# Performance work log

Hardware: AMD Instinct MI355X
Metric: run time of the kernel (lower is better)

Reference implementation:

```python
import jax, jax.numpy as jnp
import numpy as np

N_HEADS = 16
KQ_DIM = 64
EMB_DIM = 1024
CTX_DIM = 1024
EPS = 1e-5

def _layernorm(x, w, b):
    # LayerNorm over last dim (kq_dim), elementwise affine
    mu = jnp.mean(x, axis=-1, keepdims=True)
    var = jnp.mean(jnp.square(x - mu), axis=-1, keepdims=True)
    return (x - mu) * jax.lax.rsqrt(var + EPS) * w + b

def setup_inputs() -> dict:
    key = jax.random.key(0)
    ks = jax.random.split(key, 10)
    B, SQ, SK = 2, 2048, 2048
    inner = N_HEADS * KQ_DIM
    s_e = 1.0 / np.sqrt(EMB_DIM)
    s_c = 1.0 / np.sqrt(CTX_DIM)
    s_i = 1.0 / np.sqrt(inner)
    return {
        "emb": jax.random.normal(ks[0], (B, SQ, EMB_DIM), jnp.float32),
        "context": jax.random.normal(ks[1], (B, SK, CTX_DIM), jnp.float32),
        "Wq": jax.random.uniform(ks[2], (inner, EMB_DIM), jnp.float32, -s_e, s_e),
        "Wk": jax.random.uniform(ks[3], (inner, CTX_DIM), jnp.float32, -s_c, s_c),
        "Wv": jax.random.uniform(ks[4], (inner, CTX_DIM), jnp.float32, -s_c, s_c),
        "Wu": jax.random.uniform(ks[5], (EMB_DIM, inner), jnp.float32, -s_i, s_i),
        "bu": jax.random.uniform(ks[6], (EMB_DIM,), jnp.float32, -s_i, s_i),
        "qn_w": jnp.ones((KQ_DIM,), jnp.float32),
        "qn_b": jnp.zeros((KQ_DIM,), jnp.float32),
        "kn_w": jnp.ones((KQ_DIM,), jnp.float32),
        "kn_b": jnp.zeros((KQ_DIM,), jnp.float32),
    }

def reference(emb, context, Wq, Wk, Wv, Wu, bu, qn_w, qn_b, kn_w, kn_b):
    B, SQ, _ = emb.shape
    SK = context.shape[1]
    # projections (no bias), reshape to [B, H, S, D]
    q = (emb @ Wq.T).reshape(B, SQ, N_HEADS, KQ_DIM).transpose(0, 2, 1, 3)
    k = (context @ Wk.T).reshape(B, SK, N_HEADS, KQ_DIM).transpose(0, 2, 1, 3)
    v = (context @ Wv.T).reshape(B, SK, N_HEADS, KQ_DIM).transpose(0, 2, 1, 3)
    q = _layernorm(q, qn_w, qn_b)
    k = _layernorm(k, kn_w, kn_b)
    scale = 1.0 / jnp.sqrt(jnp.asarray(KQ_DIM, emb.dtype))
    attn = jnp.einsum('bhqd,bhkd->bhqk', q, k) * scale
    attn = jax.nn.softmax(attn, axis=-1)
    out = jnp.einsum('bhqk,bhkd->bhqd', attn, v)
    out = out.transpose(0, 2, 1, 3).reshape(B, SQ, N_HEADS * KQ_DIM)
    return out @ Wu.T + bu
```

## Files before the change

kernel.cpp:

```cpp
#include <hip/hip_runtime.h>


typedef __attribute__((ext_vector_type(8)))  short bf16x8;
typedef __attribute__((ext_vector_type(4)))  short bf16x4;
typedef __attribute__((ext_vector_type(4)))  float f32x4;
typedef __attribute__((ext_vector_type(16))) float f32x16;
typedef __attribute__((ext_vector_type(4)))  unsigned int u32x4;

typedef __attribute__((address_space(1))) const void cg_void;
typedef __attribute__((address_space(3))) void lds_void_t;

__device__ __forceinline__ void gl_lds16(const void* g, void* l){
  __builtin_amdgcn_global_load_lds((cg_void*)g, (lds_void_t*)l, 16, 0, 0);
}

__device__ __forceinline__ short f2b(float f){
  unsigned int u;
  __builtin_memcpy(&u, &f, 4);
  u += 0x7fffu + ((u >> 16) & 1u);
  return (short)(u >> 16);
}

__global__ __launch_bounds__(256) void cvt6_kernel(
    const float* __restrict__ emb, const float* __restrict__ ctx,
    const float* __restrict__ Wq, const float* __restrict__ Wk,
    const float* __restrict__ Wv, const float* __restrict__ Wu,
    short* __restrict__ o_emb, short* __restrict__ o_ctx,
    short* __restrict__ o_wq, short* __restrict__ o_wk,
    short* __restrict__ o_wv, short* __restrict__ o_wu)
{
  const long M1 = 1024L * 1024L, M4 = 4L * M1;
  long e = ((long)blockIdx.x * 256 + threadIdx.x) * 4;
  if (e >= 12L * M1) return;
  const float* src; short* dst; long off;
  if      (e <     M4)      { src = emb; dst = o_emb; off = e;           }
  else if (e < 2 * M4)      { src = ctx; dst = o_ctx; off = e - M4;      }
  else if (e < 2 * M4 + M1) { src = Wq;  dst = o_wq;  off = e - 2 * M4;  }
  else if (e < 2 * M4 + 2*M1){src = Wk;  dst = o_wk;  off = e - 2*M4 - M1;}
  else if (e < 2 * M4 + 3*M1){src = Wv;  dst = o_wv;  off = e - 2*M4 - 2*M1;}
  else                      { src = Wu;  dst = o_wu;  off = e - 2*M4 - 3*M1;}
  f32x4 v = *(const f32x4*)(src + off);
  bf16x4 o;
  o[0] = f2b(v[0]); o[1] = f2b(v[1]); o[2] = f2b(v[2]); o[3] = f2b(v[3]);
  *(bf16x4*)(dst + off) = o;
}

__global__ __launch_bounds__(256) void gemm_qkv_kernel(
    const short* __restrict__ embh, const short* __restrict__ ctxh,
    const short* __restrict__ Wqh, const short* __restrict__ Wkh,
    const short* __restrict__ Wvh,
    short* __restrict__ qo, short* __restrict__ ko, short* __restrict__ vto,
    const float* __restrict__ qw, const float* __restrict__ qb,
    const float* __restrict__ kw, const float* __restrict__ kb)
{
  const int K = 1024;
  __shared__ short As[128 * 64];
  __shared__ short Bs[128 * 64];
  const int tid  = threadIdx.x;
  const int wave = tid >> 6, lane = tid & 63;
  const int quad = lane >> 4, r16 = lane & 15;
  const int wm = (wave >> 1) * 64, wn = (wave & 1) * 64;

  const int task = blockIdx.y;
  int bn, bm, N;
  const short *A, *B;
  if (task == 2){
    bn = (blockIdx.x & 31) * 128; bm = (blockIdx.x >> 5) * 128; N = 4096;
    A = Wvh; B = ctxh;
  } else {
    bm = (blockIdx.x & 31) * 128; bn = (blockIdx.x >> 5) * 128; N = 1024;
    A = task ? ctxh : embh; B = task ? Wkh : Wqh;
  }

  f32x4 acc[4][4];
#pragma unroll
  for (int i = 0; i < 4; i++)
#pragma unroll
    for (int j = 0; j < 4; j++)
      acc[i][j] = (f32x4){0.f, 0.f, 0.f, 0.f};

  const int sr7 = (lane >> 3) & 7;
  const size_t arow = (size_t)(bm + wave * 8 + (lane >> 3)) * K
                      + (((lane & 7) ^ sr7) * 8);
  const size_t brow = (size_t)(bn + wave * 8 + (lane >> 3)) * K
                      + (((lane & 7) ^ sr7) * 8);

  const int sw = ((quad ^ (r16 & 7)) << 3);

  for (int k0 = 0; k0 < K; k0 += 64){
#pragma unroll
    for (int i = 0; i < 4; i++){
      gl_lds16(A + arow + (size_t)32 * i * K + k0, &As[wave * 512 + i * 2048]);
      gl_lds16(B + brow + (size_t)32 * i * K + k0, &Bs[wave * 512 + i * 2048]);
    }
    __syncthreads();
#pragma unroll
    for (int kk = 0; kk < 2; kk++){
      const int off = sw ^ (kk << 5);
      bf16x8 af[4], bq[4];
#pragma unroll
      for (int i = 0; i < 4; i++)
        af[i] = *(const bf16x8*)(&As[(wm + i*16 + r16) * 64 + off]);
#pragma unroll
      for (int j = 0; j < 4; j++)
        bq[j] = *(const bf16x8*)(&Bs[(wn + j*16 + r16) * 64 + off]);
#pragma unroll
      for (int i = 0; i < 4; i++)
#pragma unroll
        for (int j = 0; j < 4; j++)
          acc[i][j] = __builtin_amdgcn_mfma_f32_16x16x32_bf16(af[i], bq[j], acc[i][j], 0, 0, 0);
    }
    __syncthreads();
  }

  if (task < 2){
    short* Ch = task ? ko : qo;
    const float* lw = task ? kw : qw;
    const float* lb = task ? kb : qb;
    float wv[4], bv[4];
#pragma unroll
    for (int j = 0; j < 4; j++){ wv[j] = lw[j*16 + r16]; bv[j] = lb[j*16 + r16]; }
#pragma unroll
    for (int i = 0; i < 4; i++){
#pragma unroll
      for (int t = 0; t < 4; t++){
        float a[4];
#pragma unroll
        for (int j = 0; j < 4; j++) a[j] = acc[i][j][t];
        float s = a[0] + a[1] + a[2] + a[3];
        s += __shfl_xor(s, 1); s += __shfl_xor(s, 2);
        s += __shfl_xor(s, 4); s += __shfl_xor(s, 8);
        const float mu = s * 0.015625f;
        float d[4], sq = 0.f;
#pragma unroll
        for (int j = 0; j < 4; j++){ d[j] = a[j] - mu; sq += d[j]*d[j]; }
        sq += __shfl_xor(sq, 1); sq += __shfl_xor(sq, 2);
        sq += __shfl_xor(sq, 4); sq += __shfl_xor(sq, 8);
        const float si = rsqrtf(sq * 0.015625f + 1e-5f);
        const size_t row = (size_t)(bm + wm + i*16 + quad*4 + t);
#pragma unroll
        for (int j = 0; j < 4; j++)
          Ch[row * 1024 + (bn + wn + j*16 + r16)] = f2b(d[j] * si * wv[j] + bv[j]);
      }
    }
  } else {
#pragma unroll
    for (int i = 0; i < 4; i++){
#pragma unroll
      for (int j = 0; j < 4; j++){
        const int p = (r16 & 3) | ((j & 1) << 2) | (((r16 >> 2) & 1) << 3)
                      | (((r16 >> 3) & 1) << 4);
        const int col = ((bn + wn + j*16 + r16) & ~31) | p;
#pragma unroll
        for (int t = 0; t < 4; t++){
          const size_t row = (size_t)(bm + wm + i*16 + quad*4 + t);
          vto[row * (size_t)N + col] = f2b(acc[i][j][t]);
        }
      }
    }
  }
}

__global__ __launch_bounds__(512) void gemm_out_kernel(
    const short* __restrict__ A, const short* __restrict__ B,
    float* __restrict__ Cf, const float* __restrict__ bias)
{
  const int K = 1024, N = 1024;
  __shared__ short As[2][128 * 64];
  __shared__ short Bs[2][128 * 64];
  const int tid  = threadIdx.x;
  const int wave = tid >> 6, lane = tid & 63;
  const int half = wave >> 2, wg = wave & 3;
  const int quad = lane >> 4, r16 = lane & 15;
  const int wm = (wg >> 1) * 64, wn = (wg & 1) * 64;
  const int bm = blockIdx.x * 128, bn = blockIdx.y * 128;

  f32x4 acc[4][4];
#pragma unroll
  for (int i = 0; i < 4; i++)
#pragma unroll
    for (int j = 0; j < 4; j++)
      acc[i][j] = (f32x4){0.f, 0.f, 0.f, 0.f};

  const int kh = half * 512;
  const int sr7 = (lane >> 3) & 7;
  const size_t arow = (size_t)(bm + wg * 8 + (lane >> 3)) * K + kh
                      + (((lane & 7) ^ sr7) * 8);
  const size_t brow = (size_t)(bn + wg * 8 + (lane >> 3)) * K + kh
                      + (((lane & 7) ^ sr7) * 8);
  const int sw = ((quad ^ (r16 & 7)) << 3);

  for (int k0 = 0; k0 < 512; k0 += 64){
#pragma unroll
    for (int i = 0; i < 4; i++){
      gl_lds16(A + arow + (size_t)32 * i * K + k0, &As[half][wg * 512 + i * 2048]);
      gl_lds16(B + brow + (size_t)32 * i * K + k0, &Bs[half][wg * 512 + i * 2048]);
    }
    __syncthreads();
#pragma unroll
    for (int kk = 0; kk < 2; kk++){
      const int off = sw ^ (kk << 5);
      bf16x8 af[4], bq[4];
#pragma unroll
      for (int i = 0; i < 4; i++)
        af[i] = *(const bf16x8*)(&As[half][(wm + i*16 + r16) * 64 + off]);
#pragma unroll
      for (int j = 0; j < 4; j++)
        bq[j] = *(const bf16x8*)(&Bs[half][(wn + j*16 + r16) * 64 + off]);
#pragma unroll
      for (int i = 0; i < 4; i++)
#pragma unroll
        for (int j = 0; j < 4; j++)
          acc[i][j] = __builtin_amdgcn_mfma_f32_16x16x32_bf16(af[i], bq[j], acc[i][j], 0, 0, 0);
    }
    __syncthreads();
  }

  float* scr = (float*)&As[0][0];
#pragma unroll
  for (int i = 0; i < 4; i++){
    if (half == 1){
      float* p = scr + (wg * 64 + lane) * 17;
#pragma unroll
      for (int j = 0; j < 4; j++)
#pragma unroll
        for (int t = 0; t < 4; t++) p[j*4 + t] = acc[i][j][t];
    }
    __syncthreads();
    if (half == 0){
      const float* p = scr + (wg * 64 + lane) * 17;
#pragma unroll
      for (int j = 0; j < 4; j++){
        const int col = bn + wn + j*16 + r16;
#pragma unroll
        for (int t = 0; t < 4; t++){
          const size_t row = (size_t)(bm + wm + i*16 + quad*4 + t);
          Cf[row * N + col] = acc[i][j][t] + p[j*4 + t] + bias[col];
        }
      }
    }
    __syncthreads();
  }
}

__global__ __launch_bounds__(512, 4) void flash2_kernel(
    const short* __restrict__ Q, const short* __restrict__ K,
    const short* __restrict__ Vt, short* __restrict__ O)
{
  __shared__ __align__(16) long long smem8[8192];
  short* Ks  = (short*)smem8;
  short* Vts = Ks + 16384;
  float* scr = (float*)smem8;

  const int tid = threadIdx.x;
  const int wave = tid >> 6, lane = tid & 63;
  const int half = wave >> 2, wg = wave & 3;
  const int hh = lane >> 5, q5 = lane & 31;
  const int h = blockIdx.x, qb = blockIdx.y, b = blockIdx.z;
  const int q0 = qb * 128 + wg * 32;

  const size_t kbase = ((size_t)b * 2048) * 1024 + (size_t)h * 64;
  const size_t vbase = ((size_t)h * 64) * 4096 + (size_t)b * 2048;

  bf16x8 qf[4];
  {
    const size_t qrow = ((size_t)b * 2048 + q0 + q5) * 1024 + (size_t)h * 64;
#pragma unroll
    for (int c = 0; c < 4; c++)
      qf[c] = *(const bf16x8*)(Q + qrow + c * 16 + hh * 8);
  }

  f32x16 oacc[2];
#pragma unroll
  for (int mt = 0; mt < 2; mt++)
#pragma unroll
    for (int t = 0; t < 16; t++) oacc[mt][t] = 0.f;
  float lsum = 0.f;

  const int srow = lane >> 3;
  const int csrc = ((lane & 7) ^ srow) * 8;
  const int wr0 = wg * 16;

#define STAGE(bufi, kt)                                                         \
  {                                                                             \
    const short* ks = K + kbase + (size_t)((kt) * 64 + wr0 + srow) * 1024 + csrc; \
    const short* vs = Vt + vbase + (size_t)(wr0 + srow) * 4096 + (kt) * 64 + csrc; \
    short* kd = Ks  + (half * 2 + (bufi)) * 4096 + wr0 * 64;                    \
    short* vd = Vts + (half * 2 + (bufi)) * 4096 + wr0 * 64;                    \
    gl_lds16(ks,            kd);                                                \
    gl_lds16(ks + 8 * 1024, kd + 512);                                          \
    gl_lds16(vs,            vd);                                                \
    gl_lds16(vs + 8 * 4096, vd + 512);                                          \
  }

  STAGE(0, half)

  for (int i = 0; i < 16; i++){
    const int buf = i & 1;
    __syncthreads();
    if (i + 1 < 16) STAGE(buf ^ 1, 2 * (i + 1) + half)

    const short* kb_l = Ks  + (half * 2 + buf) * 4096;
    const short* vb_l = Vts + (half * 2 + buf) * 4096;

#pragma unroll
    for (int s32 = 0; s32 < 2; s32++){
      f32x16 sacc;
#pragma unroll
      for (int t = 0; t < 16; t++) sacc[t] = 0.f;
      const int key = s32 * 32 + q5;
#pragma unroll
      for (int c = 0; c < 4; c++){
        bf16x8 kf = *(const bf16x8*)(&kb_l[key * 64 + (((2*c + hh) ^ (key & 7)) << 3)]);
        sacc = __builtin_amdgcn_mfma_f32_32x32x16_bf16(kf, qf[c], sacc, 0, 0, 0);
      }

      unsigned int pu[16];
#pragma unroll
      for (int t = 0; t < 16; t++){
        const float e = __builtin_amdgcn_exp2f(sacc[t] * 0.18033688f);
        lsum += e;
        unsigned int u; __builtin_memcpy(&u, &e, 4);
        pu[t] = u + 0x8000u;
      }

#pragma unroll
      for (int c = 0; c < 2; c++){
        u32x4 tmp;
        tmp[0] = __builtin_amdgcn_perm(pu[4*c + 1], pu[4*c + 0], 0x07060302u);
        tmp[1] = __builtin_amdgcn_perm(pu[4*c + 3], pu[4*c + 2], 0x07060302u);
        tmp[2] = __builtin_amdgcn_perm(pu[8 + 4*c + 1], pu[8 + 4*c + 0], 0x07060302u);
        tmp[3] = __builtin_amdgcn_perm(pu[8 + 4*c + 3], pu[8 + 4*c + 2], 0x07060302u);
        bf16x8 pf; __builtin_memcpy(&pf, &tmp, 16);
#pragma unroll
        for (int mt = 0; mt < 2; mt++){
          const int d = mt * 32 + q5;
          bf16x8 vf = *(const bf16x8*)(&vb_l[d * 64 + (((s32*4 + 2*c + hh) ^ (d & 7)) << 3)]);
          oacc[mt] = __builtin_amdgcn_mfma_f32_32x32x16_bf16(vf, pf, oacc[mt], 0, 0, 0);
        }
      }
    }
  }

  lsum += __shfl_xor(lsum, 32);
  __syncthreads();
  float* base = scr + (wg * 64 + lane) * 33;
  if (half == 1){
#pragma unroll
    for (int t = 0; t < 16; t++){ base[t] = oacc[0][t]; base[16 + t] = oacc[1][t]; }
    scr[8448 + wg * 64 + lane] = lsum;
  }
  __syncthreads();
  if (half == 0){
    const float l2 = scr[8448 + wg * 64 + lane];
    const float linv = 1.0f / (lsum + l2);
    const size_t orow = ((size_t)b * 2048 + q0 + q5) * 1024 + (size_t)h * 64;
#pragma unroll
    for (int mt = 0; mt < 2; mt++){
#pragma unroll
      for (int g = 0; g < 4; g++){
        bf16x4 o4;
#pragma unroll
        for (int u = 0; u < 4; u++)
          o4[u] = f2b((oacc[mt][g*4 + u] + base[mt*16 + g*4 + u]) * linv);
        *(bf16x4*)(O + orow + mt*32 + g*8 + 4*hh) = o4;
      }
    }
  }
}
#undef STAGE

extern "C" void kernel_launch(void* const* d_in, const int* in_sizes, int n_in,
                              void* d_out, int out_size, void* d_ws, size_t ws_size,
                              hipStream_t stream) {
  const float* emb  = (const float*)d_in[0];
  const float* ctx  = (const float*)d_in[1];
  const float* Wq   = (const float*)d_in[2];
  const float* Wk   = (const float*)d_in[3];
  const float* Wv   = (const float*)d_in[4];
  const float* Wu   = (const float*)d_in[5];
  const float* bu   = (const float*)d_in[6];
  const float* qn_w = (const float*)d_in[7];
  const float* qn_b = (const float*)d_in[8];
  const float* kn_w = (const float*)d_in[9];
  const float* kn_b = (const float*)d_in[10];
  float* out = (float*)d_out;

  const size_t BIG = (size_t)4096 * 1024;
  const size_t WSZ = (size_t)1024 * 1024;
  short* ws   = (short*)d_ws;
  short* embh = ws;
  short* ctxh = embh + BIG;
  short* Wqh  = ctxh + BIG;
  short* Wkh  = Wqh + WSZ;
  short* Wvh  = Wkh + WSZ;
  short* Wuh  = Wvh + WSZ;
  short* qh   = Wuh + WSZ;
  short* kh   = qh + BIG;
  short* vth  = kh + BIG;
  short* aoh  = vth + BIG;

  cvt6_kernel<<<12288, 256, 0, stream>>>(emb, ctx, Wq, Wk, Wv, Wu,
                                         embh, ctxh, Wqh, Wkh, Wvh, Wuh);

  gemm_qkv_kernel<<<dim3(256, 3), 256, 0, stream>>>(
      embh, ctxh, Wqh, Wkh, Wvh, qh, kh, vth,
      qn_w, qn_b, kn_w, kn_b);

  flash2_kernel<<<dim3(16, 16, 2), 512, 0, stream>>>(qh, kh, vth, aoh);

  gemm_out_kernel<<<dim3(32, 8), 512, 0, stream>>>(aoh, Wuh, out, bu);
}
```

Baseline: 205.1 us.

## Fold softmax scale into Q layernorm, batch QK MFMAs, split out-GEMM K four ways

Three separate changes. The softmax scale (log2e/sqrt(d)) is folded into the Q layernorm weight and bias, which removes a multiply per score in the flash kernel. The flash kernel now loads all K fragments first and interleaves the two 32-key MFMA chains, giving the scheduler more independent MFMAs to overlap. The output GEMM goes from 512 threads with a 2-way K split to 1024 threads with a 4-way K split, reduced through LDS, which doubles shared memory to 128KB and may limit occupancy.

New measurement: 199.8 us. -2.6%, faster.

```diff
diff --git a/kernel.cpp b/kernel.cpp
--- a/kernel.cpp
+++ b/kernel.cpp
@@ -6,6 +6,8 @@
 typedef __attribute__((ext_vector_type(4)))  float f32x4;
 typedef __attribute__((ext_vector_type(16))) float f32x16;
 typedef __attribute__((ext_vector_type(4)))  unsigned int u32x4;
+
+#define SM_SCALE 0.18033688f
 
 typedef __attribute__((address_space(1))) const void cg_void;
 typedef __attribute__((address_space(3))) void lds_void_t;
@@ -84,7 +86,6 @@
                       + (((lane & 7) ^ sr7) * 8);
   const size_t brow = (size_t)(bn + wave * 8 + (lane >> 3)) * K
                       + (((lane & 7) ^ sr7) * 8);
-
   const int sw = ((quad ^ (r16 & 7)) << 3);
 
   for (int k0 = 0; k0 < K; k0 += 64){
@@ -117,9 +118,13 @@
     short* Ch = task ? ko : qo;
     const float* lw = task ? kw : qw;
     const float* lb = task ? kb : qb;
+    const float post = task ? 1.0f : SM_SCALE;
     float wv[4], bv[4];
 #pragma unroll
-    for (int j = 0; j < 4; j++){ wv[j] = lw[j*16 + r16]; bv[j] = lb[j*16 + r16]; }
+    for (int j = 0; j < 4; j++){
+      wv[j] = lw[j*16 + r16] * post;
+      bv[j] = lb[j*16 + r16] * post;
+    }
 #pragma unroll
     for (int i = 0; i < 4; i++){
 #pragma unroll
@@ -161,16 +166,16 @@
   }
 }
 
-__global__ __launch_bounds__(512) void gemm_out_kernel(
+__global__ __launch_bounds__(1024, 4) void gemm_out_kernel(
     const short* __restrict__ A, const short* __restrict__ B,
     float* __restrict__ Cf, const float* __restrict__ bias)
 {
   const int K = 1024, N = 1024;
-  __shared__ short As[2][128 * 64];
-  __shared__ short Bs[2][128 * 64];
+  __shared__ short As[4][128 * 64];
+  __shared__ short Bs[4][128 * 64];
   const int tid  = threadIdx.x;
   const int wave = tid >> 6, lane = tid & 63;
-  const int half = wave >> 2, wg = wave & 3;
+  const int qt = wave >> 2, wg = wave & 3;
   const int quad = lane >> 4, r16 = lane & 15;
   const int wm = (wg >> 1) * 64, wn = (wg & 1) * 64;
   const int bm = blockIdx.x * 128, bn = blockIdx.y * 128;
@@ -182,7 +187,7 @@
     for (int j = 0; j < 4; j++)
       acc[i][j] = (f32x4){0.f, 0.f, 0.f, 0.f};
 
-  const int kh = half * 512;
+  const int kh = qt * 256;
   const int sr7 = (lane >> 3) & 7;
   const size_t arow = (size_t)(bm + wg * 8 + (lane >> 3)) * K + kh
                       + (((lane & 7) ^ sr7) * 8);
@@ -190,11 +195,11 @@
                       + (((lane & 7) ^ sr7) * 8);
   const int sw = ((quad ^ (r16 & 7)) << 3);
 
-  for (int k0 = 0; k0 < 512; k0 += 64){
+  for (int k0 = 0; k0 < 256; k0 += 64){
 #pragma unroll
     for (int i = 0; i < 4; i++){
-      gl_lds16(A + arow + (size_t)32 * i * K + k0, &As[half][wg * 512 + i * 2048]);
-      gl_lds16(B + brow + (size_t)32 * i * K + k0, &Bs[half][wg * 512 + i * 2048]);
+      gl_lds16(A + arow + (size_t)32 * i * K + k0, &As[qt][wg * 512 + i * 2048]);
+      gl_lds16(B + brow + (size_t)32 * i * K + k0, &Bs[qt][wg * 512 + i * 2048]);
     }
     __syncthreads();
 #pragma unroll
@@ -203,10 +208,10 @@
       bf16x8 af[4], bq[4];
 #pragma unroll
       for (int i = 0; i < 4; i++)
-        af[i] = *(const bf16x8*)(&As[half][(wm + i*16 + r16) * 64 + off]);
+        af[i] = *(const bf16x8*)(&As[qt][(wm + i*16 + r16) * 64 + off]);
 #pragma unroll
       for (int j = 0; j < 4; j++)
-        bq[j] = *(const bf16x8*)(&Bs[half][(wn + j*16 + r16) * 64 + off]);
+        bq[j] = *(const bf16x8*)(&Bs[qt][(wn + j*16 + r16) * 64 + off]);
 #pragma unroll
       for (int i = 0; i < 4; i++)
 #pragma unroll
@@ -219,23 +224,26 @@
   float* scr = (float*)&As[0][0];
 #pragma unroll
   for (int i = 0; i < 4; i++){
-    if (half == 1){
-      float* p = scr + (wg * 64 + lane) * 17;
+    if (qt != 0){
+      float* p = scr + ((qt - 1) * 256 + wg * 64 + lane) * 17;
 #pragma unroll
       for (int j = 0; j < 4; j++)
 #pragma unroll
         for (int t = 0; t < 4; t++) p[j*4 + t] = acc[i][j][t];
     }
     __syncthreads();
-    if (half == 0){
-      const float* p = scr + (wg * 64 + lane) * 17;
+    if (qt == 0){
+      const float* p0 = scr + (wg * 64 + lane) * 17;
+      const float* p1 = p0 + 256 * 17;
+      const float* p2 = p1 + 256 * 17;
 #pragma unroll
       for (int j = 0; j < 4; j++){
         const int col = bn + wn + j*16 + r16;
 #pragma unroll
         for (int t = 0; t < 4; t++){
           const size_t row = (size_t)(bm + wm + i*16 + quad*4 + t);
-          Cf[row * N + col] = acc[i][j][t] + p[j*4 + t] + bias[col];
+          Cf[row * N + col] = acc[i][j][t] + p0[j*4+t] + p1[j*4+t] + p2[j*4+t]
+                              + bias[col];
         }
       }
     }
@@ -303,22 +311,29 @@
     const short* kb_l = Ks  + (half * 2 + buf) * 4096;
     const short* vb_l = Vts + (half * 2 + buf) * 4096;
 
+    bf16x8 kf[2][4];
 #pragma unroll
     for (int s32 = 0; s32 < 2; s32++){
-      f32x16 sacc;
-#pragma unroll
-      for (int t = 0; t < 16; t++) sacc[t] = 0.f;
       const int key = s32 * 32 + q5;
 #pragma unroll
-      for (int c = 0; c < 4; c++){
-        bf16x8 kf = *(const bf16x8*)(&kb_l[key * 64 + (((2*c + hh) ^ (key & 7)) << 3)]);
-        sacc = __builtin_amdgcn_mfma_f32_32x32x16_bf16(kf, qf[c], sacc, 0, 0, 0);
-      }
-
+      for (int c = 0; c < 4; c++)
+        kf[s32][c] = *(const bf16x8*)(&kb_l[key * 64 + (((2*c + hh) ^ (key & 7)) << 3)]);
+    }
+    f32x16 sacc[2];
+#pragma unroll
+    for (int t = 0; t < 16; t++){ sacc[0][t] = 0.f; sacc[1][t] = 0.f; }
+#pragma unroll
+    for (int c = 0; c < 4; c++){
+      sacc[0] = __builtin_amdgcn_mfma_f32_32x32x16_bf16(kf[0][c], qf[c], sacc[0], 0, 0, 0);
+      sacc[1] = __builtin_amdgcn_mfma_f32_32x32x16_bf16(kf[1][c], qf[c], sacc[1], 0, 0, 0);
+    }
+
+#pragma unroll
+    for (int s32 = 0; s32 < 2; s32++){
       unsigned int pu[16];
 #pragma unroll
       for (int t = 0; t < 16; t++){
-        const float e = __builtin_amdgcn_exp2f(sacc[t] * 0.18033688f);
+        const float e = __builtin_amdgcn_exp2f(sacc[s32][t]);
         lsum += e;
         unsigned int u; __builtin_memcpy(&u, &e, 4);
         pu[t] = u + 0x8000u;
@@ -409,5 +424,5 @@
 
   flash2_kernel<<<dim3(16, 16, 2), 512, 0, stream>>>(qh, kh, vth, aoh);
 
-  gemm_out_kernel<<<dim3(32, 8), 512, 0, stream>>>(aoh, Wuh, out, bu);
-}
+  gemm_out_kernel<<<dim3(32, 8), 1024, 0, stream>>>(aoh, Wuh, out, bu);
+}
```
